# Optimization experiments

Hardware: AMD Instinct MI355X
Metric: run time of the kernel (lower is better)

Reference implementation:

```python
import jax, jax.numpy as jnp
import numpy as np

B, T, S, E, H = 4, 32, 256, 512, 8
D = E // H
SCALE = np.sqrt(D).astype(np.float32)
Q_MOD, K_MOD = 0, 1


def setup_inputs() -> dict:
    key = jax.random.key(0)
    ks = jax.random.split(key, 12)
    def spikes(k):
        return (jax.random.uniform(k, (B, T, S, E)) < 0.1).astype(jnp.float32)
    init = lambda k, shp: jax.random.normal(k, shp, dtype=jnp.float32) * (1.0 / np.sqrt(shp[0]))
    return {
        "query_spikes": spikes(ks[0]),
        "key_spikes": spikes(ks[1]),
        "value_spikes": spikes(ks[2]),
        "Wq": init(ks[3], (E, E)), "bq": jnp.zeros((E,), jnp.float32),
        "Wk": init(ks[4], (E, E)), "bk": jnp.zeros((E,), jnp.float32),
        "Wv": init(ks[5], (E, E)), "bv": jnp.zeros((E,), jnp.float32),
        "Wo": init(ks[6], (E, E)), "bo": jnp.zeros((E,), jnp.float32),
        "modality_weights": jnp.ones((2, H), jnp.float32),          # nn.Parameter(torch.ones(2, num_heads))
        "temporal_sync": jax.random.normal(ks[7], (T, H), jnp.float32) * 0.1,  # torch.randn(T, H) * 0.1
    }


def _spike_softmax(scores):
    # sigmoid((s - max)*5) normalized along key axis
    m = jnp.max(scores, axis=-1, keepdims=True)
    p = jax.nn.sigmoid((scores - m) * 5.0)
    return p / (jnp.sum(p, axis=-1, keepdims=True) + 1e-8)


def reference(query_spikes, key_spikes, value_spikes, Wq, bq, Wk, bk, Wv, bv, Wo, bo,
              modality_weights, temporal_sync):
    def proj(x, W, b):  # [B,T,S,E] -> [B,T,H,S,D]
        y = jnp.einsum("btse,ef->btsf", x, W) + b
        return y.reshape(B, T, S, H, D).transpose(0, 1, 3, 2, 4)

    Q = proj(query_spikes, Wq, bq)
    K = proj(key_spikes, Wk, bk)
    V = proj(value_spikes, Wv, bv)

    # attention scores across all timesteps at once: [B,T,H,Sq,Sk]
    scores = jnp.einsum("bthqd,bthkd->bthqk", Q, K) / SCALE
    mod_w = (modality_weights[Q_MOD] * modality_weights[K_MOD]).reshape(1, 1, H, 1, 1)
    scores = scores * mod_w + temporal_sync.reshape(1, T, H, 1, 1)

    attn = _spike_softmax(scores)
    attended = jnp.einsum("bthqk,bthkd->bthqd", attn, V)   # [B,T,H,Sq,D]
    attended = attended.transpose(0, 1, 3, 2, 4).reshape(B, T, S, E)
    return jnp.einsum("btse,ef->btsf", attended, Wo) + bo
```

## Files before the change

kernel.cpp:

```cpp
#include <hip/hip_runtime.h>
#include <hip/hip_bf16.h>

#define DI __device__ __forceinline__

typedef __bf16 bf16x8 __attribute__((ext_vector_type(8)));
typedef float  f32x4  __attribute__((ext_vector_type(4)));
typedef float  f32x16 __attribute__((ext_vector_type(16)));


DI ushort f2bf(float f) {
  union { float f; unsigned u; } v; v.f = f;
  unsigned r = v.u + 0x7fffu + ((v.u >> 16) & 1u);
  return (ushort)(r >> 16);
}

DI unsigned cvtpk2(float a, float b) {
  unsigned r;
  asm("v_cvt_pk_bf16_f32 %0, %1, %2" : "=v"(r) : "v"(a), "v"(b));
  return r;
}

DI float rcpf(float x) {
  float r;
  asm("v_rcp_f32 %0, %1" : "=v"(r) : "v"(x));
  return r;
}

DI void gload_lds16(const void* g, void* lds) {
  __builtin_amdgcn_global_load_lds(
      (const __attribute__((address_space(1))) unsigned*)g,
      (__attribute__((address_space(3))) unsigned*)lds, 16, 0, 0);
}

#define WAITVM8   asm volatile("s_waitcnt vmcnt(8)" ::: "memory")
#define WAITVM4   asm volatile("s_waitcnt vmcnt(4)" ::: "memory")
#define WAITVM0   asm volatile("s_waitcnt vmcnt(0)" ::: "memory")
#define WAITLGKM0 asm volatile("s_waitcnt lgkmcnt(0)" ::: "memory")
#define SBAR      __builtin_amdgcn_s_barrier()

DI f32x4 zero4() { f32x4 z; z[0] = 0.f; z[1] = 0.f; z[2] = 0.f; z[3] = 0.f; return z; }

DI f32x16 zero16() {
  f32x16 z;
  for (int i = 0; i < 16; i++) z[i] = 0.f;
  return z;
}

union BF8U { ushort u[8]; unsigned d[4]; bf16x8 v; };

__global__ __launch_bounds__(256) void wtrans_kernel(
    const float* __restrict__ W0, const float* __restrict__ W1,
    const float* __restrict__ W2, const float* __restrict__ W3,
    ushort* __restrict__ out) {
  __shared__ float tile[64][65];
  const float* W = blockIdx.z == 0 ? W0 : blockIdx.z == 1 ? W1 : blockIdx.z == 2 ? W2 : W3;
  ushort* o = out + (size_t)blockIdx.z * 512 * 512;
  int k0 = blockIdx.x * 64, n0 = blockIdx.y * 64;
  int tid = threadIdx.x;
#pragma unroll
  for (int i = 0; i < 16; i++) {
    int idx = i * 256 + tid; int r = idx >> 6, c = idx & 63;
    tile[r][c] = W[(size_t)(k0 + r) * 512 + n0 + c];
  }
  __syncthreads();
#pragma unroll
  for (int i = 0; i < 16; i++) {
    int idx = i * 256 + tid; int r = idx >> 6, c = idx & 63;
    o[(size_t)(n0 + r) * 512 + k0 + c] = f2bf(tile[c][r]);
  }
}

__global__ __launch_bounds__(256) void bitpack_kernel(
    const float* __restrict__ q, const float* __restrict__ k,
    const float* __restrict__ v, unsigned char* __restrict__ bits) {
  const float* src = blockIdx.y == 0 ? q : blockIdx.y == 1 ? k : v;
  unsigned char* dst = bits + (size_t)blockIdx.y * 2097152;
  for (int g = blockIdx.x * 256 + threadIdx.x; g < 2097152; g += 2048 * 256) {
    int m = g >> 6, j = g & 63, sub = j >> 3, t = j & 7;
    const uint4* p = (const uint4*)(src + (size_t)m * 512 + t * 64 + sub * 8);
    uint4 a = p[0], b = p[1];
    unsigned byte = 0;
    byte |= (a.x != 0u) << 0; byte |= (a.y != 0u) << 1;
    byte |= (a.z != 0u) << 2; byte |= (a.w != 0u) << 3;
    byte |= (b.x != 0u) << 4; byte |= (b.y != 0u) << 5;
    byte |= (b.z != 0u) << 6; byte |= (b.w != 0u) << 7;
    dst[g] = (unsigned char)byte;
  }
}

__global__ __launch_bounds__(256, 2) void qkv_gemm_kernel(
    const unsigned char* __restrict__ Abits, const ushort* __restrict__ Wt,
    const float* __restrict__ bqp, const float* __restrict__ bkp,
    const float* __restrict__ bvp,
    ushort* __restrict__ Qw, ushort* __restrict__ Kw, ushort* __restrict__ Vt) {
  __shared__ __align__(16) char Alds[32768];
  __shared__ __align__(16) char Blds[32768];
  int z = blockIdx.z;
  const unsigned char* Ab8 = Abits + (size_t)z * 2097152;
  const ushort* Bt = Wt + (size_t)z * 262144;
  const float* bias = z == 0 ? bqp : z == 1 ? bkp : bvp;
  int bl = ((int)blockIdx.x & 7) * 128 + ((int)blockIdx.x >> 3);
  int m0 = (bl >> 2) * 128, n0 = (bl & 3) * 128;
  int tid = threadIdx.x, lane = tid & 63, wv = tid >> 6;
  int wm = (wv >> 1) * 64, wn = (wv & 1) * 64;
  int srow = tid >> 3, skg = tid & 7;

  f32x4 acc[4][4];
#pragma unroll
  for (int i = 0; i < 4; i++)
#pragma unroll
    for (int j = 0; j < 4; j++) acc[i][j] = zero4();

  uint2 bits[4];
#pragma unroll
  for (int rr = 0; rr < 4; rr++)
    bits[rr] = *(const uint2*)(Ab8 + (size_t)(m0 + srow + rr * 32) * 64 + skg * 8);

  auto writeA = [&](int t) {
    char* Ad = Alds + (t & 1) * 16384;
#pragma unroll
    for (int rr = 0; rr < 4; rr++) {
      int r = srow + rr * 32;
      unsigned byte = ((t < 4 ? bits[rr].x >> (8 * t) : bits[rr].y >> (8 * (t - 4)))) & 255u;
      BF8U av;
#pragma unroll
      for (int b = 0; b < 8; b++) av.u[b] = (byte >> b) & 1u ? (ushort)0x3F80 : (ushort)0;
      *(bf16x8*)(Ad + ((r * 128 + skg * 16) ^ ((r & 7) << 4))) = av.v;
    }
  };
  auto issueB = [&](int t) {
    char* Bb = Blds + (t & 1) * 16384;
#pragma unroll
    for (int i = 0; i < 4; i++) {
      int c = (wv * 4 + i) * 64 + lane;
      int r = c >> 3, g = (c & 7) ^ (r & 7);
      gload_lds16(Bt + (size_t)(n0 + r) * 512 + t * 64 + g * 8, Bb + (wv * 4 + i) * 1024);
    }
  };
  auto compute = [&](int t) {
    char* Ad = Alds + (t & 1) * 16384;
    char* Bb = Blds + (t & 1) * 16384;
#pragma unroll
    for (int ks = 0; ks < 2; ks++) {
      bf16x8 a[4], b[4];
#pragma unroll
      for (int i = 0; i < 4; i++) {
        int ra = wm + i * 16 + (lane & 15);
        a[i] = *(const bf16x8*)(Ad + ((ra * 128 + (ks * 4 + (lane >> 4)) * 16) ^ ((ra & 7) << 4)));
        int rb = wn + i * 16 + (lane & 15);
        b[i] = *(const bf16x8*)(Bb + ((rb * 128 + (ks * 4 + (lane >> 4)) * 16) ^ ((rb & 7) << 4)));
      }
#pragma unroll
      for (int i = 0; i < 4; i++)
#pragma unroll
        for (int j = 0; j < 4; j++)
          acc[i][j] = __builtin_amdgcn_mfma_f32_16x16x32_bf16(a[i], b[j], acc[i][j], 0, 0, 0);
    }
  };

  writeA(0); issueB(0); issueB(1);
  WAITLGKM0;

#pragma unroll
  for (int t = 0; t < 8; t++) {
    if (t < 7) { WAITVM4; } else { WAITVM0; }
    SBAR;
    compute(t);
    if (t < 7) writeA(t + 1);
    WAITLGKM0;
    SBAR;
    if (t < 6) issueB(t + 2);
  }

#pragma unroll
  for (int j = 0; j < 4; j++) {
    int col = n0 + wn + j * 16 + (lane & 15);
    float bv = bias[col];
#pragma unroll
    for (int i = 0; i < 4; i++) {
      int row0 = m0 + wm + i * 16 + (lane >> 4) * 4;
      if (z == 2) {
        int btv = row0 >> 8, s = row0 & 255;
        ushort4 w;
        w.x = f2bf(acc[i][j][0] + bv); w.y = f2bf(acc[i][j][1] + bv);
        w.z = f2bf(acc[i][j][2] + bv); w.w = f2bf(acc[i][j][3] + bv);
        *(ushort4*)(Vt + ((size_t)btv * 512 + col) * 256 + s) = w;
      } else {
        ushort* C = z == 0 ? Qw : Kw;
#pragma unroll
        for (int r = 0; r < 4; r++)
          C[(size_t)(row0 + r) * 512 + col] = f2bf(acc[i][j][r] + bv);
      }
    }
  }
}

__global__ __launch_bounds__(256, 2) void out_gemm_kernel(
    const ushort* __restrict__ A, const ushort* __restrict__ Bt,
    const float* __restrict__ bias, float* __restrict__ C) {
  __shared__ __align__(16) char Alds[32768];
  __shared__ __align__(16) char Blds[32768];
  int bl = ((int)blockIdx.x & 7) * 128 + ((int)blockIdx.x >> 3);
  int m0 = (bl >> 2) * 128, n0 = (bl & 3) * 128;
  int tid = threadIdx.x, lane = tid & 63, wv = tid >> 6;
  int wm = (wv >> 1) * 64, wn = (wv & 1) * 64;

  f32x4 acc[4][4];
#pragma unroll
  for (int i = 0; i < 4; i++)
#pragma unroll
    for (int j = 0; j < 4; j++) acc[i][j] = zero4();

  auto stage = [&](int t) {
    char* Ab = Alds + (t & 1) * 16384;
    char* Bb = Blds + (t & 1) * 16384;
#pragma unroll
    for (int i = 0; i < 4; i++) {
      int c = (wv * 4 + i) * 64 + lane;
      int r = c >> 3, g = (c & 7) ^ (r & 7);
      gload_lds16(A + (size_t)(m0 + r) * 512 + t * 64 + g * 8, Ab + (wv * 4 + i) * 1024);
      gload_lds16(Bt + (size_t)(n0 + r) * 512 + t * 64 + g * 8, Bb + (wv * 4 + i) * 1024);
    }
  };
  auto compute = [&](int t) {
    char* Ab = Alds + (t & 1) * 16384;
    char* Bb = Blds + (t & 1) * 16384;
#pragma unroll
    for (int ks = 0; ks < 2; ks++) {
      bf16x8 a[4], b[4];
#pragma unroll
      for (int i = 0; i < 4; i++) {
        int ra = wm + i * 16 + (lane & 15);
        a[i] = *(const bf16x8*)(Ab + ((ra * 128 + (ks * 4 + (lane >> 4)) * 16) ^ ((ra & 7) << 4)));
        int rb = wn + i * 16 + (lane & 15);
        b[i] = *(const bf16x8*)(Bb + ((rb * 128 + (ks * 4 + (lane >> 4)) * 16) ^ ((rb & 7) << 4)));
      }
#pragma unroll
      for (int i = 0; i < 4; i++)
#pragma unroll
        for (int j = 0; j < 4; j++)
          acc[i][j] = __builtin_amdgcn_mfma_f32_16x16x32_bf16(a[i], b[j], acc[i][j], 0, 0, 0);
    }
  };

  stage(0);
  stage(1);
#pragma unroll
  for (int t = 0; t < 8; t++) {
    if (t < 7) { WAITVM8; } else { WAITVM0; }
    SBAR;
    compute(t);
    WAITLGKM0;
    SBAR;
    if (t < 6) stage(t + 2);
  }

  int lane2 = threadIdx.x & 63;
#pragma unroll
  for (int j = 0; j < 4; j++) {
    int col = n0 + wn + j * 16 + (lane2 & 15);
    float bv = bias[col];
#pragma unroll
    for (int i = 0; i < 4; i++) {
      int row0 = m0 + wm + i * 16 + (lane2 >> 4) * 4;
#pragma unroll
      for (int r = 0; r < 4; r++)
        C[(size_t)(row0 + r) * 512 + col] = acc[i][j][r] + bv;
    }
  }
}

__global__ __launch_bounds__(256) void attn_kernel(
    const ushort* __restrict__ Q, const ushort* __restrict__ K,
    const ushort* __restrict__ Vt, const float* __restrict__ mw,
    ushort* __restrict__ att) {
  __shared__ __align__(16) char Klds[32768];
  __shared__ __align__(16) char Vlds[32768];
  int tid = threadIdx.x, lane = tid & 63, wv = tid >> 6;
  int lq = lane & 31, hi = lane >> 5;
  int b = blockIdx.x;
  int h = b & 7, bt = b >> 3;
  const ushort* Qb = Q + ((size_t)bt * 256 + wv * 64) * 512 + h * 64;
  const ushort* Kb = K + ((size_t)bt * 256) * 512 + h * 64;
  const ushort* Vb = Vt + ((size_t)bt * 512 + h * 64) * 256;
  float c0 = mw[h] * mw[8 + h] * 0.125f;

#pragma unroll
  for (int i = 0; i < 8; i++) {
    int ci = (wv * 8 + i) * 64 + lane;
    int l2 = ci & 31, h2 = (ci >> 5) & 1, ds = (ci >> 6) & 3, kt = ci >> 8;
    gload_lds16(Kb + (size_t)(kt * 32 + l2) * 512 + ds * 16 + h2 * 8,
                &Klds[(wv * 8 + i) * 1024]);
  }
  bf16x8 qf[2][4];
#pragma unroll
  for (int qj = 0; qj < 2; qj++)
#pragma unroll
    for (int ds = 0; ds < 4; ds++)
      qf[qj][ds] = *(const bf16x8*)(Qb + (size_t)(qj * 32 + lq) * 512 + ds * 16 + hi * 8);
  __syncthreads();

#pragma unroll
  for (int i = 0; i < 8; i++) {
    int ci = (wv * 8 + i) * 64 + lane;
    int l2 = ci & 31, h2 = (ci >> 5) & 1, df = (ci >> 6) & 1, ks = (ci >> 7) & 1, kt = ci >> 8;
    gload_lds16(Vb + (size_t)(df * 32 + l2) * 256 + kt * 32 + ks * 16 + h2 * 8,
                &Vlds[(wv * 8 + i) * 1024]);
  }

  float mx[2] = {-3.0e38f, -3.0e38f};
#pragma unroll 2
  for (int kt = 0; kt < 8; kt++) {
    bf16x8 kf[4];
#pragma unroll
    for (int ds = 0; ds < 4; ds++)
      kf[ds] = *(const bf16x8*)(&Klds[((kt * 4 + ds) * 2 + hi) * 512 + lq * 16]);
#pragma unroll
    for (int qj = 0; qj < 2; qj++) {
      f32x16 sT = zero16();
#pragma unroll
      for (int ds = 0; ds < 4; ds++)
        sT = __builtin_amdgcn_mfma_f32_32x32x16_bf16(kf[ds], qf[qj][ds], sT, 0, 0, 0);
#pragma unroll
      for (int r = 0; r < 16; r++) mx[qj] = fmaxf(mx[qj], sT[r] * c0);
    }
  }
#pragma unroll
  for (int qj = 0; qj < 2; qj++) mx[qj] = fmaxf(mx[qj], __shfl_xor(mx[qj], 32, 64));
  __syncthreads();

  float a5 = 5.f * c0;
  float m5[2] = {5.f * mx[0], 5.f * mx[1]};
  float sm[2] = {0.f, 0.f};
  f32x16 acc[2][2];
  acc[0][0] = zero16(); acc[0][1] = zero16(); acc[1][0] = zero16(); acc[1][1] = zero16();

#pragma unroll 2
  for (int kt = 0; kt < 8; kt++) {
    bf16x8 kf[4], vf[2][2];
#pragma unroll
    for (int ds = 0; ds < 4; ds++)
      kf[ds] = *(const bf16x8*)(&Klds[((kt * 4 + ds) * 2 + hi) * 512 + lq * 16]);
#pragma unroll
    for (int ks = 0; ks < 2; ks++)
#pragma unroll
      for (int df = 0; df < 2; df++)
        vf[ks][df] = *(const bf16x8*)(&Vlds[(((kt * 2 + ks) * 2 + df) * 2 + hi) * 512 + lq * 16]);
#pragma unroll
    for (int qj = 0; qj < 2; qj++) {
      f32x16 sT = zero16();
#pragma unroll
      for (int ds = 0; ds < 4; ds++)
        sT = __builtin_amdgcn_mfma_f32_32x32x16_bf16(kf[ds], qf[qj][ds], sT, 0, 0, 0);
      unsigned pk[8];
#pragma unroll
      for (int i = 0; i < 8; i++) {
        float p0 = rcpf(1.f + __expf(m5[qj] - sT[2 * i] * a5));
        float p1 = rcpf(1.f + __expf(m5[qj] - sT[2 * i + 1] * a5));
        sm[qj] += p0 + p1;
        pk[i] = cvtpk2(p0, p1);
      }
#pragma unroll
      for (int ks = 0; ks < 2; ks++) {
        int bb = ks * 4;
        unsigned sa = (unsigned)__shfl_xor((int)pk[bb + 0], 32, 64);
        unsigned sb = (unsigned)__shfl_xor((int)pk[bb + 1], 32, 64);
        unsigned sc = (unsigned)__shfl_xor((int)pk[bb + 2], 32, 64);
        unsigned sd = (unsigned)__shfl_xor((int)pk[bb + 3], 32, 64);
        BF8U pa;
        pa.d[0] = hi ? sc : pk[bb + 0];
        pa.d[1] = hi ? sd : pk[bb + 1];
        pa.d[2] = hi ? pk[bb + 2] : sa;
        pa.d[3] = hi ? pk[bb + 3] : sb;
#pragma unroll
        for (int df = 0; df < 2; df++)
          acc[qj][df] = __builtin_amdgcn_mfma_f32_32x32x16_bf16(pa.v, vf[ks][df], acc[qj][df], 0, 0, 0);
      }
    }
  }

#pragma unroll
  for (int qj = 0; qj < 2; qj++) sm[qj] += __shfl_xor(sm[qj], 32, 64);
  float rs[2] = {rcpf(sm[0] + 1e-8f), rcpf(sm[1] + 1e-8f)};
#pragma unroll
  for (int qj = 0; qj < 2; qj++) {
#pragma unroll
    for (int r = 0; r < 16; r++) {
      int ql = (r & 3) + 8 * (r >> 2) + 4 * hi;
      float rr = __shfl(rs[qj], ql, 64);
      size_t rowbase = ((size_t)bt * 256 + wv * 64 + qj * 32 + ql) * 512 + h * 64;
#pragma unroll
      for (int df = 0; df < 2; df++)
        att[rowbase + df * 32 + lq] = f2bf(acc[qj][df][r] * rr);
    }
  }
}

extern "C" void kernel_launch(void* const* d_in, const int* in_sizes, int n_in,
                              void* d_out, int out_size, void* d_ws, size_t ws_size,
                              hipStream_t stream) {
  (void)in_sizes; (void)n_in; (void)out_size; (void)ws_size;
  const float* qs  = (const float*)d_in[0];
  const float* ksn = (const float*)d_in[1];
  const float* vsn = (const float*)d_in[2];
  const float* Wq  = (const float*)d_in[3];
  const float* bq  = (const float*)d_in[4];
  const float* Wk  = (const float*)d_in[5];
  const float* bk  = (const float*)d_in[6];
  const float* Wv  = (const float*)d_in[7];
  const float* bv  = (const float*)d_in[8];
  const float* Wo  = (const float*)d_in[9];
  const float* bo  = (const float*)d_in[10];
  const float* mw  = (const float*)d_in[11];

  char* ws = (char*)d_ws;
  const size_t SLOT = 33554432u;
  ushort* Wt = (ushort*)ws;
  unsigned char* Abits = (unsigned char*)(ws + (size_t)(2u << 20));
  char*   s0 = ws + (size_t)(8u << 20);
  ushort* Qw = (ushort*)(s0 + 0 * SLOT);
  ushort* Kw = (ushort*)(s0 + 1 * SLOT);
  ushort* Vt = (ushort*)(s0 + 2 * SLOT);
  ushort* Aw = (ushort*)(s0 + 3 * SLOT);

  wtrans_kernel<<<dim3(8, 8, 4), 256, 0, stream>>>(Wq, Wk, Wv, Wo, Wt);
  bitpack_kernel<<<dim3(2048, 3), 256, 0, stream>>>(qs, ksn, vsn, Abits);
  qkv_gemm_kernel<<<dim3(1024, 1, 3), 256, 0, stream>>>(Abits, Wt, bq, bk, bv,
                                                        Qw, Kw, Vt);
  attn_kernel<<<dim3(1024), 256, 0, stream>>>(Qw, Kw, Vt, mw, Aw);
  out_gemm_kernel<<<dim3(1024), 256, 0, stream>>>(Aw, Wt + 3 * 262144, bo, (float*)d_out);
}
```

Before: 214.2 us.

## Expand bit-packed A fragments directly in registers, dropping A shared-memory staging

The QKV GEMM now has each lane load the packed spike bits for its own MFMA A-fragment rows and expand them to bf16 in registers, instead of writing expanded tiles to LDS and reading them back. This removes the A LDS buffer, its writes and reads, and halves shared memory use. Launch bounds rise to 4 blocks per CU to exploit the freed LDS. The cost is redundant bit expansion across waves sharing rows, more VALU work inside the compute loop, and register pressure under the tighter occupancy bound.

```diff
diff --git a/kernel.cpp b/kernel.cpp
--- a/kernel.cpp
+++ b/kernel.cpp
@@ -88,12 +88,11 @@
   }
 }
 
-__global__ __launch_bounds__(256, 2) void qkv_gemm_kernel(
+__global__ __launch_bounds__(256, 4) void qkv_gemm_kernel(
     const unsigned char* __restrict__ Abits, const ushort* __restrict__ Wt,
     const float* __restrict__ bqp, const float* __restrict__ bkp,
     const float* __restrict__ bvp,
     ushort* __restrict__ Qw, ushort* __restrict__ Kw, ushort* __restrict__ Vt) {
-  __shared__ __align__(16) char Alds[32768];
   __shared__ __align__(16) char Blds[32768];
   int z = blockIdx.z;
   const unsigned char* Ab8 = Abits + (size_t)z * 2097152;
@@ -103,7 +102,7 @@
   int m0 = (bl >> 2) * 128, n0 = (bl & 3) * 128;
   int tid = threadIdx.x, lane = tid & 63, wv = tid >> 6;
   int wm = (wv >> 1) * 64, wn = (wv & 1) * 64;
-  int srow = tid >> 3, skg = tid & 7;
+  int hi4 = lane >> 4;
 
   f32x4 acc[4][4];
 #pragma unroll
@@ -111,22 +110,20 @@
 #pragma unroll
     for (int j = 0; j < 4; j++) acc[i][j] = zero4();
 
-  uint2 bits[4];
-#pragma unroll
-  for (int rr = 0; rr < 4; rr++)
-    bits[rr] = *(const uint2*)(Ab8 + (size_t)(m0 + srow + rr * 32) * 64 + skg * 8);
-
-  auto writeA = [&](int t) {
-    char* Ad = Alds + (t & 1) * 16384;
-#pragma unroll
-    for (int rr = 0; rr < 4; rr++) {
-      int r = srow + rr * 32;
-      unsigned byte = ((t < 4 ? bits[rr].x >> (8 * t) : bits[rr].y >> (8 * (t - 4)))) & 255u;
-      BF8U av;
-#pragma unroll
-      for (int b = 0; b < 8; b++) av.u[b] = (byte >> b) & 1u ? (ushort)0x3F80 : (ushort)0;
-      *(bf16x8*)(Ad + ((r * 128 + skg * 16) ^ ((r & 7) << 4))) = av.v;
-    }
+  uint2 abits[4][2];
+#pragma unroll
+  for (int i = 0; i < 4; i++)
+#pragma unroll
+    for (int ks = 0; ks < 2; ks++)
+      abits[i][ks] = *(const uint2*)(Ab8 + (size_t)(m0 + wm + i * 16 + (lane & 15)) * 64
+                                     + (ks * 4 + hi4) * 8);
+
+  auto expandA = [&](int i, int ks, int t) -> bf16x8 {
+    unsigned w = t < 4 ? abits[i][ks].x >> (8 * t) : abits[i][ks].y >> (8 * (t - 4));
+    BF8U av;
+#pragma unroll
+    for (int b = 0; b < 8; b++) av.u[b] = (w >> b) & 1u ? (ushort)0x3F80 : (ushort)0;
+    return av.v;
   };
   auto issueB = [&](int t) {
     char* Bb = Blds + (t & 1) * 16384;
@@ -138,17 +135,15 @@
     }
   };
   auto compute = [&](int t) {
-    char* Ad = Alds + (t & 1) * 16384;
     char* Bb = Blds + (t & 1) * 16384;
 #pragma unroll
     for (int ks = 0; ks < 2; ks++) {
       bf16x8 a[4], b[4];
 #pragma unroll
       for (int i = 0; i < 4; i++) {
-        int ra = wm + i * 16 + (lane & 15);
-        a[i] = *(const bf16x8*)(Ad + ((ra * 128 + (ks * 4 + (lane >> 4)) * 16) ^ ((ra & 7) << 4)));
         int rb = wn + i * 16 + (lane & 15);
-        b[i] = *(const bf16x8*)(Bb + ((rb * 128 + (ks * 4 + (lane >> 4)) * 16) ^ ((rb & 7) << 4)));
+        b[i] = *(const bf16x8*)(Bb + ((rb * 128 + (ks * 4 + hi4) * 16) ^ ((rb & 7) << 4)));
+        a[i] = expandA(i, ks, t);
       }
 #pragma unroll
       for (int i = 0; i < 4; i++)
@@ -158,15 +153,12 @@
     }
   };
 
-  writeA(0); issueB(0); issueB(1);
-  WAITLGKM0;
-
+  issueB(0); issueB(1);
 #pragma unroll
   for (int t = 0; t < 8; t++) {
     if (t < 7) { WAITVM4; } else { WAITVM0; }
     SBAR;
     compute(t);
-    if (t < 7) writeA(t + 1);
     WAITLGKM0;
     SBAR;
     if (t < 6) issueB(t + 2);
```

After: 196.1 us. -8.5%, faster.
